# Kernel optimization log

Measured on AMD Instinct MI355X. Metric: run time of the kernel, lower is better.

## Reference

```python
import jax, jax.numpy as jnp
import numpy as np

N_NODES = 100000
N_EDGES = 1600000
IN_DIM, HID_DIM, N_CLASSES = 128, 64, 40


def spmm(edge_row, edge_col, edge_val, dense):
    # sparse [N,N] @ dense [N,D] via gather + segment-sum over edges
    msgs = edge_val[:, None] * dense[edge_col]            # [E, D]
    return jax.ops.segment_sum(msgs, edge_row, num_segments=N_NODES)


def setup_inputs() -> dict:
    key = jax.random.key(0)
    ks = jax.random.split(key, 8)
    x = jax.random.normal(ks[0], (N_NODES, IN_DIM), dtype=jnp.float32)
    edge_row = jax.random.randint(ks[1], (N_EDGES,), 0, N_NODES, dtype=jnp.int32)
    edge_col = jax.random.randint(ks[2], (N_EDGES,), 0, N_NODES, dtype=jnp.int32)
    edge_val = jax.random.uniform(ks[3], (N_EDGES,), dtype=jnp.float32)
    s1 = 1.0 / np.sqrt(IN_DIM)
    s2 = 1.0 / np.sqrt(HID_DIM)
    W1 = jax.random.normal(ks[4], (IN_DIM, HID_DIM), dtype=jnp.float32) * s1
    b1 = jnp.zeros((HID_DIM,), dtype=jnp.float32)
    W2 = jax.random.normal(ks[5], (HID_DIM, HID_DIM), dtype=jnp.float32) * s2
    b2 = jnp.zeros((HID_DIM,), dtype=jnp.float32)
    Wc = jax.random.normal(ks[6], (HID_DIM, N_CLASSES), dtype=jnp.float32) * s2
    bc = jnp.zeros((N_CLASSES,), dtype=jnp.float32)
    return {"x": x, "edge_row": edge_row, "edge_col": edge_col, "edge_val": edge_val,
            "W1": W1, "b1": b1, "W2": W2, "b2": b2, "Wc": Wc, "bc": bc}


def reference(x, edge_row, edge_col, edge_val, W1, b1, W2, b2, Wc, bc):
    # GCN layer 1: support = xW+b, aggregate, relu  (dropout off in eval)
    h = jax.nn.relu(spmm(edge_row, edge_col, edge_val, x @ W1 + b1))
    # GCN layer 2
    h = spmm(edge_row, edge_col, edge_val, h @ W2 + b2)
    # node classifier + log-softmax
    logits = h @ Wc + bc
    return jax.nn.log_softmax(logits, axis=-1)
```

## Files before the change

### kernel.cpp

```cpp
#include <hip/hip_runtime.h>

#define N_NODES   100000
#define N_EDGES   1600000
#define IN_DIM    128
#define HID_DIM   64
#define N_CLASSES 40

#define NBUCK 782
#define BCAP  2816
#define EPB   6400
#define PBLK  1024

typedef __attribute__((ext_vector_type(8))) short bf16x8;
typedef __attribute__((ext_vector_type(4))) float f32x4;

__device__ inline short f2bf(float f) {
    unsigned u = __float_as_uint(f);
    unsigned r = (u + 0x7FFFu + ((u >> 16) & 1u)) >> 16;
    return (short)r;
}
__device__ inline float bflo(unsigned w) { return __uint_as_float(w << 16); }
__device__ inline float bfhi(unsigned w) { return __uint_as_float(w & 0xFFFF0000u); }
__device__ inline float upval(unsigned w) { return __uint_as_float((w >> 17) << 16); }

__global__ __launch_bounds__(256) void prep_weights(const float* __restrict__ W1,
                                                    const float* __restrict__ W2,
                                                    const float* __restrict__ Wc,
                                                    const float* __restrict__ b2,
                                                    short* __restrict__ W1t,
                                                    short* __restrict__ Mt,
                                                    float* __restrict__ bv,
                                                    int* __restrict__ bcnt) {
    for (int i = blockIdx.x * 256 + threadIdx.x; i < IN_DIM * HID_DIM; i += gridDim.x * 256) {
        int n = i >> 7, k = i & 127;
        W1t[i] = f2bf(W1[k * HID_DIM + n]);
    }
    if (blockIdx.x == 7) {
        for (int i = threadIdx.x; i < NBUCK; i += 256) bcnt[i] = 0;
    }
    if (blockIdx.x == 0) {
        for (int idx = threadIdx.x; idx < HID_DIM * HID_DIM; idx += 256) {
            int n = idx >> 6, i = idx & 63;
            float acc = 0.f;
            if (n < N_CLASSES)
                for (int j = 0; j < HID_DIM; ++j)
                    acc = fmaf(W2[i * HID_DIM + j], Wc[j * N_CLASSES + n], acc);
            Mt[n * HID_DIM + i] = f2bf(acc);
        }
        for (int n = threadIdx.x; n < N_CLASSES; n += 256) {
            float acc = 0.f;
            for (int j = 0; j < HID_DIM; ++j)
                acc = fmaf(b2[j], Wc[j * N_CLASSES + n], acc);
            bv[n] = acc;
        }
    }
}

__global__ __launch_bounds__(256) void gemm1_mfma(const float* __restrict__ x,
                                                  const short* __restrict__ W1t,
                                                  const float* __restrict__ b1,
                                                  unsigned short* __restrict__ out) {
    int wave = threadIdx.x >> 6;
    int lane = threadIdx.x & 63;
    int node0 = blockIdx.x * 64 + wave * 16;
    if (node0 >= N_NODES) return;
    int m = lane & 15;
    int q = lane >> 4;
    const float* xrow = x + (size_t)(node0 + m) * IN_DIM;
    f32x4 acc0 = {0,0,0,0}, acc1 = {0,0,0,0}, acc2 = {0,0,0,0}, acc3 = {0,0,0,0};
#pragma unroll
    for (int kb = 0; kb < 4; ++kb) {
        int k0 = kb * 32 + q * 8;
        float4 a0 = *(const float4*)(xrow + k0);
        float4 a1 = *(const float4*)(xrow + k0 + 4);
        bf16x8 af;
        af[0]=f2bf(a0.x); af[1]=f2bf(a0.y); af[2]=f2bf(a0.z); af[3]=f2bf(a0.w);
        af[4]=f2bf(a1.x); af[5]=f2bf(a1.y); af[6]=f2bf(a1.z); af[7]=f2bf(a1.w);
        bf16x8 bf0 = *(const bf16x8*)(W1t + ( 0 + m) * IN_DIM + k0);
        bf16x8 bf1 = *(const bf16x8*)(W1t + (16 + m) * IN_DIM + k0);
        bf16x8 bf2 = *(const bf16x8*)(W1t + (32 + m) * IN_DIM + k0);
        bf16x8 bf3 = *(const bf16x8*)(W1t + (48 + m) * IN_DIM + k0);
        acc0 = __builtin_amdgcn_mfma_f32_16x16x32_bf16(af, bf0, acc0, 0, 0, 0);
        acc1 = __builtin_amdgcn_mfma_f32_16x16x32_bf16(af, bf1, acc1, 0, 0, 0);
        acc2 = __builtin_amdgcn_mfma_f32_16x16x32_bf16(af, bf2, acc2, 0, 0, 0);
        acc3 = __builtin_amdgcn_mfma_f32_16x16x32_bf16(af, bf3, acc3, 0, 0, 0);
    }
    f32x4 accs[4] = {acc0, acc1, acc2, acc3};
#pragma unroll
    for (int t = 0; t < 4; ++t) {
        float bias = b1[t * 16 + m];
#pragma unroll
        for (int r = 0; r < 4; ++r) {
            int node = node0 + q * 4 + r;
            out[(size_t)node * HID_DIM + t * 16 + m] = (unsigned short)f2bf(accs[t][r] + bias);
        }
    }
}

__global__ __launch_bounds__(256) void gemm2u_mfma(const unsigned short* __restrict__ h,
                                                   const short* __restrict__ Mt,
                                                   unsigned short* __restrict__ out) {
    int wave = threadIdx.x >> 6;
    int lane = threadIdx.x & 63;
    int node0 = blockIdx.x * 64 + wave * 16;
    if (node0 >= N_NODES) return;
    int m = lane & 15;
    int q = lane >> 4;
    const unsigned short* hrow = h + (size_t)(node0 + m) * HID_DIM;
    f32x4 acc0 = {0,0,0,0}, acc1 = {0,0,0,0}, acc2 = {0,0,0,0}, acc3 = {0,0,0,0};
#pragma unroll
    for (int kb = 0; kb < 2; ++kb) {
        int k0 = kb * 32 + q * 8;
        bf16x8 af = *(const bf16x8*)(hrow + k0);
#pragma unroll
        for (int j = 0; j < 8; ++j)
            af[j] = ((unsigned short)af[j] & 0x8000u) ? 0 : af[j];
        bf16x8 bf0 = *(const bf16x8*)(Mt + ( 0 + m) * HID_DIM + k0);
        bf16x8 bf1 = *(const bf16x8*)(Mt + (16 + m) * HID_DIM + k0);
        bf16x8 bf2 = *(const bf16x8*)(Mt + (32 + m) * HID_DIM + k0);
        bf16x8 bf3 = *(const bf16x8*)(Mt + (48 + m) * HID_DIM + k0);
        acc0 = __builtin_amdgcn_mfma_f32_16x16x32_bf16(af, bf0, acc0, 0, 0, 0);
        acc1 = __builtin_amdgcn_mfma_f32_16x16x32_bf16(af, bf1, acc1, 0, 0, 0);
        acc2 = __builtin_amdgcn_mfma_f32_16x16x32_bf16(af, bf2, acc2, 0, 0, 0);
        acc3 = __builtin_amdgcn_mfma_f32_16x16x32_bf16(af, bf3, acc3, 0, 0, 0);
    }
    f32x4 accs[4] = {acc0, acc1, acc2, acc3};
#pragma unroll
    for (int t = 0; t < 4; ++t) {
#pragma unroll
        for (int r = 0; r < 4; ++r) {
            int node = node0 + q * 4 + r;
            out[(size_t)node * HID_DIM + t * 16 + m] = (unsigned short)f2bf(accs[t][r]);
        }
    }
}

__global__ __launch_bounds__(PBLK) void part_a(const int* __restrict__ erow,
                                               const int* __restrict__ ecol,
                                               const float* __restrict__ eval,
                                               int* __restrict__ bcnt,
                                               int2* __restrict__ tmp) {
    __shared__ int2 pay[EPB];
    __shared__ unsigned short sbuck[EPB];
    __shared__ int hist[NBUCK], lbase[NBUCK], cur[NBUCK], dofs[NBUCK], scan[NBUCK];
    int e0 = blockIdx.x * EPB;
    int tid = threadIdx.x;
    for (int i = tid; i < NBUCK; i += PBLK) { hist[i] = 0; cur[i] = 0; }
    __syncthreads();
    for (int i = tid; i < EPB; i += PBLK)
        atomicAdd(&hist[erow[e0 + i] >> 7], 1);
    __syncthreads();
    for (int i = tid; i < NBUCK; i += PBLK) {
        int n = hist[i];
        dofs[i] = i * BCAP + (n ? atomicAdd(&bcnt[i], n) : 0);
        scan[i] = n;
    }
    __syncthreads();
    for (int off = 1; off < NBUCK; off <<= 1) {
        int t = 0;
        if (tid < NBUCK && tid >= off) t = scan[tid - off];
        __syncthreads();
        if (tid < NBUCK) scan[tid] += t;
        __syncthreads();
    }
    if (tid < NBUCK) {
        lbase[tid] = scan[tid] - hist[tid];
        dofs[tid] -= lbase[tid];
    }
    __syncthreads();
    for (int i = tid; i < EPB; i += PBLK) {
        int e = e0 + i;
        int r = erow[e];
        int b = r >> 7;
        int p = lbase[b] + atomicAdd(&cur[b], 1);
        pay[p] = make_int2(((r & 127) << 17) | ecol[e], __float_as_int(eval[e]));
        sbuck[p] = (unsigned short)b;
    }
    __syncthreads();
    for (int p = tid; p < EPB; p += PBLK) {
        int b = sbuck[p];
        int dest = dofs[b] + p;
        if (dest < (b + 1) * BCAP)
            tmp[dest] = pay[p];
    }
}

__global__ __launch_bounds__(256) void part_b(const int* __restrict__ bcnt,
                                              const int2* __restrict__ tmp,
                                              unsigned* __restrict__ tmp2,
                                              int2* __restrict__ rowmeta) {
    __shared__ int2 ein[BCAP];
    __shared__ unsigned eout[BCAP];
    __shared__ int hist[128], pad[128], basep[128], cur[128], scan[128];
    int b = blockIdx.x;
    int nb = bcnt[b]; if (nb > BCAP) nb = BCAP;
    for (int i = threadIdx.x; i < nb; i += 256) ein[i] = tmp[(size_t)b * BCAP + i];
    if (threadIdx.x < 128) { hist[threadIdx.x] = 0; cur[threadIdx.x] = 0; }
    __syncthreads();
    for (int i = threadIdx.x; i < nb; i += 256)
        atomicAdd(&hist[(ein[i].x >> 17) & 127], 1);
    __syncthreads();
    if (threadIdx.x < 128) {
        pad[threadIdx.x] = (hist[threadIdx.x] + 7) & ~7;
        scan[threadIdx.x] = pad[threadIdx.x];
    }
    __syncthreads();
    for (int off = 1; off < 128; off <<= 1) {
        int t = 0;
        if (threadIdx.x < 128 && threadIdx.x >= off) t = scan[threadIdx.x - off];
        __syncthreads();
        if (threadIdx.x < 128) scan[threadIdx.x] += t;
        __syncthreads();
    }
    if (threadIdx.x < 128) basep[threadIdx.x] = scan[threadIdx.x] - pad[threadIdx.x];
    __syncthreads();
    int ntot = scan[127]; if (ntot > BCAP) ntot = BCAP;
    for (int i = threadIdx.x; i < nb; i += 256) {
        int lr = (ein[i].x >> 17) & 127;
        int p = basep[lr] + atomicAdd(&cur[lr], 1);
        if (p < BCAP) {
            unsigned u = (unsigned)ein[i].y;
            unsigned vb = ((u + 0x7FFFu + ((u >> 16) & 1u)) >> 16) & 0x7FFFu;
            eout[p] = (vb << 17) | (unsigned)(ein[i].x & 0x1FFFF);
        }
    }
    __syncthreads();
    if (threadIdx.x < 128) {
        int pe = basep[threadIdx.x] + pad[threadIdx.x];
        for (int p = basep[threadIdx.x] + hist[threadIdx.x]; p < pe && p < BCAP; ++p)
            eout[p] = 0u;
    }
    __syncthreads();
    for (int i = threadIdx.x; i < ntot; i += 256) tmp2[(size_t)b * BCAP + i] = eout[i];
    if (threadIdx.x < 128) {
        int r = b * 128 + threadIdx.x;
        if (r < N_NODES)
            rowmeta[r] = make_int2(b * BCAP + basep[threadIdx.x], pad[threadIdx.x]);
    }
}

__global__ __launch_bounds__(256) void spmm_csr(const int2* __restrict__ rowmeta,
                                                const unsigned* __restrict__ ecv,
                                                const unsigned short* __restrict__ dense,
                                                unsigned short* __restrict__ out) {
    __shared__ unsigned lm[4][8][68];
    int wave = threadIdx.x >> 6;
    int lane = threadIdx.x & 63;
    int s = lane >> 3, dq = lane & 7;
    int r = (blockIdx.x * 4 + wave) * 8 + s;
    int2 meta = rowmeta[r];
    int beg = meta.x, deg = meta.y;
    int degc = deg < 64 ? deg : 64;
    for (int e = dq; e < degc; e += 8)
        lm[wave][s][e] = ecv[beg + e];
    __syncthreads();
    const unsigned* mp = lm[wave][s];
    float a0=0,a1=0,a2=0,a3=0,a4=0,a5=0,a6=0,a7=0;
    if (deg > 0) {
        uint4 w = *(const uint4*)mp;
        for (int e = 0; e < degc; e += 4) {
            uint4 wn = (e + 4 < degc) ? *(const uint4*)(mp + e + 4) : w;
            uint4 g0 = *(const uint4*)(dense + ((size_t)(w.x & 0x1FFFF) << 6) + (dq << 3));
            uint4 g1 = *(const uint4*)(dense + ((size_t)(w.y & 0x1FFFF) << 6) + (dq << 3));
            uint4 g2 = *(const uint4*)(dense + ((size_t)(w.z & 0x1FFFF) << 6) + (dq << 3));
            uint4 g3 = *(const uint4*)(dense + ((size_t)(w.w & 0x1FFFF) << 6) + (dq << 3));
            float v0 = upval(w.x), v1 = upval(w.y), v2 = upval(w.z), v3 = upval(w.w);
            a0=fmaf(v0,bflo(g0.x),a0); a1=fmaf(v0,bfhi(g0.x),a1); a2=fmaf(v0,bflo(g0.y),a2); a3=fmaf(v0,bfhi(g0.y),a3);
            a4=fmaf(v0,bflo(g0.z),a4); a5=fmaf(v0,bfhi(g0.z),a5); a6=fmaf(v0,bflo(g0.w),a6); a7=fmaf(v0,bfhi(g0.w),a7);
            a0=fmaf(v1,bflo(g1.x),a0); a1=fmaf(v1,bfhi(g1.x),a1); a2=fmaf(v1,bflo(g1.y),a2); a3=fmaf(v1,bfhi(g1.y),a3);
            a4=fmaf(v1,bflo(g1.z),a4); a5=fmaf(v1,bfhi(g1.z),a5); a6=fmaf(v1,bflo(g1.w),a6); a7=fmaf(v1,bfhi(g1.w),a7);
            a0=fmaf(v2,bflo(g2.x),a0); a1=fmaf(v2,bfhi(g2.x),a1); a2=fmaf(v2,bflo(g2.y),a2); a3=fmaf(v2,bfhi(g2.y),a3);
            a4=fmaf(v2,bflo(g2.z),a4); a5=fmaf(v2,bfhi(g2.z),a5); a6=fmaf(v2,bflo(g2.w),a6); a7=fmaf(v2,bfhi(g2.w),a7);
            a0=fmaf(v3,bflo(g3.x),a0); a1=fmaf(v3,bfhi(g3.x),a1); a2=fmaf(v3,bflo(g3.y),a2); a3=fmaf(v3,bfhi(g3.y),a3);
            a4=fmaf(v3,bflo(g3.z),a4); a5=fmaf(v3,bfhi(g3.z),a5); a6=fmaf(v3,bflo(g3.w),a6); a7=fmaf(v3,bfhi(g3.w),a7);
            w = wn;
        }
        for (int e = 64; e < deg; ++e) {
            unsigned we = ecv[beg + e];
            uint4 g = *(const uint4*)(dense + ((size_t)(we & 0x1FFFF) << 6) + (dq << 3));
            float v = upval(we);
            a0=fmaf(v,bflo(g.x),a0); a1=fmaf(v,bfhi(g.x),a1); a2=fmaf(v,bflo(g.y),a2); a3=fmaf(v,bfhi(g.y),a3);
            a4=fmaf(v,bflo(g.z),a4); a5=fmaf(v,bfhi(g.z),a5); a6=fmaf(v,bflo(g.w),a6); a7=fmaf(v,bfhi(g.w),a7);
        }
    }
    uint4 o;
    o.x = (unsigned short)f2bf(a0) | ((unsigned)(unsigned short)f2bf(a1) << 16);
    o.y = (unsigned short)f2bf(a2) | ((unsigned)(unsigned short)f2bf(a3) << 16);
    o.z = (unsigned short)f2bf(a4) | ((unsigned)(unsigned short)f2bf(a5) << 16);
    o.w = (unsigned short)f2bf(a6) | ((unsigned)(unsigned short)f2bf(a7) << 16);
    *(uint4*)(out + (size_t)r * HID_DIM + (dq << 3)) = o;
}

__global__ __launch_bounds__(256) void spmm_cls(const int2* __restrict__ rowmeta,
                                                const unsigned* __restrict__ ecv,
                                                const unsigned short* __restrict__ dense,
                                                const float* __restrict__ bv,
                                                const float* __restrict__ bc,
                                                float* __restrict__ outF) {
    __shared__ unsigned lm[4][8][68];
    int wave = threadIdx.x >> 6;
    int lane = threadIdx.x & 63;
    int s = lane >> 3, dq = lane & 7;
    int r = (blockIdx.x * 4 + wave) * 8 + s;
    float4 bv0 = {0,0,0,0}, bv1 = {0,0,0,0}, bc0 = {0,0,0,0}, bc1 = {0,0,0,0};
    if (dq < 5) {
        bv0 = *(const float4*)(bv + dq * 8);  bv1 = *(const float4*)(bv + dq * 8 + 4);
        bc0 = *(const float4*)(bc + dq * 8);  bc1 = *(const float4*)(bc + dq * 8 + 4);
    }
    int2 meta = rowmeta[r];
    int beg = meta.x, deg = meta.y;
    int degc = deg < 64 ? deg : 64;
    for (int e = dq; e < degc; e += 8)
        lm[wave][s][e] = ecv[beg + e];
    __syncthreads();
    const unsigned* mp = lm[wave][s];
    float a0=0,a1=0,a2=0,a3=0,a4=0,a5=0,a6=0,a7=0, asum=0;
    if (deg > 0) {
        uint4 w = *(const uint4*)mp;
        for (int e = 0; e < degc; e += 4) {
            uint4 wn = (e + 4 < degc) ? *(const uint4*)(mp + e + 4) : w;
            uint4 g0 = *(const uint4*)(dense + ((size_t)(w.x & 0x1FFFF) << 6) + (dq << 3));
            uint4 g1 = *(const uint4*)(dense + ((size_t)(w.y & 0x1FFFF) << 6) + (dq << 3));
            uint4 g2 = *(const uint4*)(dense + ((size_t)(w.z & 0x1FFFF) << 6) + (dq << 3));
            uint4 g3 = *(const uint4*)(dense + ((size_t)(w.w & 0x1FFFF) << 6) + (dq << 3));
            float v0 = upval(w.x), v1 = upval(w.y), v2 = upval(w.z), v3 = upval(w.w);
            asum += v0 + v1 + v2 + v3;
            a0=fmaf(v0,bflo(g0.x),a0); a1=fmaf(v0,bfhi(g0.x),a1); a2=fmaf(v0,bflo(g0.y),a2); a3=fmaf(v0,bfhi(g0.y),a3);
            a4=fmaf(v0,bflo(g0.z),a4); a5=fmaf(v0,bfhi(g0.z),a5); a6=fmaf(v0,bflo(g0.w),a6); a7=fmaf(v0,bfhi(g0.w),a7);
            a0=fmaf(v1,bflo(g1.x),a0); a1=fmaf(v1,bfhi(g1.x),a1); a2=fmaf(v1,bflo(g1.y),a2); a3=fmaf(v1,bfhi(g1.y),a3);
            a4=fmaf(v1,bflo(g1.z),a4); a5=fmaf(v1,bfhi(g1.z),a5); a6=fmaf(v1,bflo(g1.w),a6); a7=fmaf(v1,bfhi(g1.w),a7);
            a0=fmaf(v2,bflo(g2.x),a0); a1=fmaf(v2,bfhi(g2.x),a1); a2=fmaf(v2,bflo(g2.y),a2); a3=fmaf(v2,bfhi(g2.y),a3);
            a4=fmaf(v2,bflo(g2.z),a4); a5=fmaf(v2,bfhi(g2.z),a5); a6=fmaf(v2,bflo(g2.w),a6); a7=fmaf(v2,bfhi(g2.w),a7);
            a0=fmaf(v3,bflo(g3.x),a0); a1=fmaf(v3,bfhi(g3.x),a1); a2=fmaf(v3,bflo(g3.y),a2); a3=fmaf(v3,bfhi(g3.y),a3);
            a4=fmaf(v3,bflo(g3.z),a4); a5=fmaf(v3,bfhi(g3.z),a5); a6=fmaf(v3,bflo(g3.w),a6); a7=fmaf(v3,bfhi(g3.w),a7);
            w = wn;
        }
        for (int e = 64; e < deg; ++e) {
            unsigned we = ecv[beg + e];
            uint4 g = *(const uint4*)(dense + ((size_t)(we & 0x1FFFF) << 6) + (dq << 3));
            float v = upval(we);
            asum += v;
            a0=fmaf(v,bflo(g.x),a0); a1=fmaf(v,bfhi(g.x),a1); a2=fmaf(v,bflo(g.y),a2); a3=fmaf(v,bfhi(g.y),a3);
            a4=fmaf(v,bflo(g.z),a4); a5=fmaf(v,bfhi(g.z),a5); a6=fmaf(v,bflo(g.w),a6); a7=fmaf(v,bfhi(g.w),a7);
        }
    }
    float l0 = fmaf(asum, bv0.x, a0) + bc0.x;
    float l1 = fmaf(asum, bv0.y, a1) + bc0.y;
    float l2 = fmaf(asum, bv0.z, a2) + bc0.z;
    float l3 = fmaf(asum, bv0.w, a3) + bc0.w;
    float l4 = fmaf(asum, bv1.x, a4) + bc1.x;
    float l5 = fmaf(asum, bv1.y, a5) + bc1.y;
    float l6 = fmaf(asum, bv1.z, a6) + bc1.z;
    float l7 = fmaf(asum, bv1.w, a7) + bc1.w;
    float mx = -1e30f;
    if (dq < 5)
        mx = fmaxf(fmaxf(fmaxf(l0, l1), fmaxf(l2, l3)),
                   fmaxf(fmaxf(l4, l5), fmaxf(l6, l7)));
#pragma unroll
    for (int off = 1; off < 8; off <<= 1) mx = fmaxf(mx, __shfl_xor(mx, off));
    float ss = 0.f;
    if (dq < 5)
        ss = __expf(l0 - mx) + __expf(l1 - mx) + __expf(l2 - mx) + __expf(l3 - mx)
           + __expf(l4 - mx) + __expf(l5 - mx) + __expf(l6 - mx) + __expf(l7 - mx);
#pragma unroll
    for (int off = 1; off < 8; off <<= 1) ss += __shfl_xor(ss, off);
    float lse = mx + __logf(ss);
    if (dq < 5) {
        float4 o0 = {l0 - lse, l1 - lse, l2 - lse, l3 - lse};
        float4 o1 = {l4 - lse, l5 - lse, l6 - lse, l7 - lse};
        float* dst = outF + (size_t)r * N_CLASSES + dq * 8;
        *(float4*)(dst) = o0;
        *(float4*)(dst + 4) = o1;
    }
}

extern "C" void kernel_launch(void* const* d_in, const int* in_sizes, int n_in,
                              void* d_out, int out_size, void* d_ws, size_t ws_size,
                              hipStream_t stream) {
    const float* x    = (const float*)d_in[0];
    const int*   erow = (const int*)  d_in[1];
    const int*   ecol = (const int*)  d_in[2];
    const float* eval = (const float*)d_in[3];
    const float* W1   = (const float*)d_in[4];
    const float* b1   = (const float*)d_in[5];
    const float* W2   = (const float*)d_in[6];
    const float* b2   = (const float*)d_in[7];
    const float* Wc   = (const float*)d_in[8];
    const float* bc   = (const float*)d_in[9];
    float* out = (float*)d_out;

    char* ws = (char*)d_ws;
    size_t off = 0;
    auto alloc = [&](size_t bytes) { char* p = ws + off; off += (bytes + 255) & ~(size_t)255; return p; };
    unsigned short* bufA = (unsigned short*)alloc((size_t)N_NODES * HID_DIM * sizeof(short));
    unsigned short* bufB = (unsigned short*)alloc((size_t)N_NODES * HID_DIM * sizeof(short));
    int2*     tmp     = (int2*)    alloc((size_t)NBUCK * BCAP * sizeof(int2));
    unsigned* tmp2    = (unsigned*)alloc((size_t)NBUCK * BCAP * sizeof(unsigned));
    int2*     rowmeta = (int2*)    alloc((size_t)N_NODES * sizeof(int2));
    int*      bcnt    = (int*)     alloc(NBUCK * sizeof(int));
    short*    W1t     = (short*)   alloc((size_t)IN_DIM * HID_DIM * sizeof(short));
    short*    Mt      = (short*)   alloc((size_t)HID_DIM * HID_DIM * sizeof(short));
    float*    bv      = (float*)   alloc(64 * sizeof(float));

    const int tile_grid = (N_NODES + 63) / 64;
    const int spmm_grid = N_NODES / 32;
    const int grid_a    = (N_EDGES + EPB - 1) / EPB;

    prep_weights<<<8, 256, 0, stream>>>(W1, W2, Wc, b2, W1t, Mt, bv, bcnt);
    part_a<<<grid_a, PBLK, 0, stream>>>(erow, ecol, eval, bcnt, tmp);
    part_b<<<NBUCK, 256, 0, stream>>>(bcnt, tmp, tmp2, rowmeta);

    gemm1_mfma<<<tile_grid, 256, 0, stream>>>(x, W1t, b1, bufA);
    spmm_csr<<<spmm_grid, 256, 0, stream>>>(rowmeta, tmp2, bufA, bufB);
    gemm2u_mfma<<<tile_grid, 256, 0, stream>>>(bufB, Mt, bufA);
    spmm_cls<<<spmm_grid, 256, 0, stream>>>(rowmeta, tmp2, bufA, bv, bc, out);
}
```

Before: 268.1 us.

## Fuse bucket-sort second pass with first GEMM into one launch

```diff
diff --git a/kernel.cpp b/kernel.cpp
--- a/kernel.cpp
+++ b/kernel.cpp
@@ -10,6 +10,7 @@
 #define BCAP  2816
 #define EPB   6400
 #define PBLK  1024
+#define G1BLK 1563
 
 typedef __attribute__((ext_vector_type(8))) short bf16x8;
 typedef __attribute__((ext_vector_type(4))) float f32x4;
@@ -56,43 +57,149 @@
     }
 }
 
-__global__ __launch_bounds__(256) void gemm1_mfma(const float* __restrict__ x,
-                                                  const short* __restrict__ W1t,
-                                                  const float* __restrict__ b1,
-                                                  unsigned short* __restrict__ out) {
-    int wave = threadIdx.x >> 6;
-    int lane = threadIdx.x & 63;
-    int node0 = blockIdx.x * 64 + wave * 16;
-    if (node0 >= N_NODES) return;
-    int m = lane & 15;
-    int q = lane >> 4;
-    const float* xrow = x + (size_t)(node0 + m) * IN_DIM;
-    f32x4 acc0 = {0,0,0,0}, acc1 = {0,0,0,0}, acc2 = {0,0,0,0}, acc3 = {0,0,0,0};
-#pragma unroll
-    for (int kb = 0; kb < 4; ++kb) {
-        int k0 = kb * 32 + q * 8;
-        float4 a0 = *(const float4*)(xrow + k0);
-        float4 a1 = *(const float4*)(xrow + k0 + 4);
-        bf16x8 af;
-        af[0]=f2bf(a0.x); af[1]=f2bf(a0.y); af[2]=f2bf(a0.z); af[3]=f2bf(a0.w);
-        af[4]=f2bf(a1.x); af[5]=f2bf(a1.y); af[6]=f2bf(a1.z); af[7]=f2bf(a1.w);
-        bf16x8 bf0 = *(const bf16x8*)(W1t + ( 0 + m) * IN_DIM + k0);
-        bf16x8 bf1 = *(const bf16x8*)(W1t + (16 + m) * IN_DIM + k0);
-        bf16x8 bf2 = *(const bf16x8*)(W1t + (32 + m) * IN_DIM + k0);
-        bf16x8 bf3 = *(const bf16x8*)(W1t + (48 + m) * IN_DIM + k0);
-        acc0 = __builtin_amdgcn_mfma_f32_16x16x32_bf16(af, bf0, acc0, 0, 0, 0);
-        acc1 = __builtin_amdgcn_mfma_f32_16x16x32_bf16(af, bf1, acc1, 0, 0, 0);
-        acc2 = __builtin_amdgcn_mfma_f32_16x16x32_bf16(af, bf2, acc2, 0, 0, 0);
-        acc3 = __builtin_amdgcn_mfma_f32_16x16x32_bf16(af, bf3, acc3, 0, 0, 0);
-    }
-    f32x4 accs[4] = {acc0, acc1, acc2, acc3};
-#pragma unroll
-    for (int t = 0; t < 4; ++t) {
-        float bias = b1[t * 16 + m];
-#pragma unroll
-        for (int r = 0; r < 4; ++r) {
-            int node = node0 + q * 4 + r;
-            out[(size_t)node * HID_DIM + t * 16 + m] = (unsigned short)f2bf(accs[t][r] + bias);
+__global__ __launch_bounds__(PBLK) void part_a(const int* __restrict__ erow,
+                                               const int* __restrict__ ecol,
+                                               const float* __restrict__ eval,
+                                               int* __restrict__ bcnt,
+                                               int2* __restrict__ tmp) {
+    __shared__ int2 pay[EPB];
+    __shared__ int hist[NBUCK], lbase[NBUCK], cur[NBUCK], dofs[NBUCK], scan[NBUCK];
+    int e0 = blockIdx.x * EPB;
+    int tid = threadIdx.x;
+    for (int i = tid; i < NBUCK; i += PBLK) { hist[i] = 0; cur[i] = 0; }
+    __syncthreads();
+    for (int i = tid; i < EPB; i += PBLK)
+        atomicAdd(&hist[erow[e0 + i] >> 7], 1);
+    __syncthreads();
+    for (int i = tid; i < NBUCK; i += PBLK) {
+        int n = hist[i];
+        dofs[i] = i * BCAP + (n ? atomicAdd(&bcnt[i], n) : 0);
+        scan[i] = n;
+    }
+    __syncthreads();
+    for (int off = 1; off < NBUCK; off <<= 1) {
+        int t = 0;
+        if (tid < NBUCK && tid >= off) t = scan[tid - off];
+        __syncthreads();
+        if (tid < NBUCK) scan[tid] += t;
+        __syncthreads();
+    }
+    if (tid < NBUCK) {
+        lbase[tid] = scan[tid] - hist[tid];
+        dofs[tid] -= lbase[tid];
+    }
+    __syncthreads();
+    for (int i = tid; i < EPB; i += PBLK) {
+        int e = e0 + i;
+        int r = erow[e];
+        int b = r >> 7;
+        int p = lbase[b] + atomicAdd(&cur[b], 1);
+        unsigned u = __float_as_uint(eval[e]);
+        unsigned vb = ((u + 0x7FFFu + ((u >> 16) & 1u)) >> 16) & 0x7FFFu;
+        pay[p] = make_int2(((r & 127) << 17) | ecol[e], (int)((vb << 10) | (unsigned)b));
+    }
+    __syncthreads();
+    for (int p = tid; p < EPB; p += PBLK) {
+        int2 v = pay[p];
+        int b = (unsigned)v.y & 1023u;
+        int dest = dofs[b] + p;
+        if (dest < (b + 1) * BCAP)
+            tmp[dest] = v;
+    }
+}
+
+__global__ __launch_bounds__(256) void part_b_gemm1(const int* __restrict__ bcnt,
+                                                    const int2* __restrict__ tmp,
+                                                    unsigned* __restrict__ tmp2,
+                                                    int2* __restrict__ rowmeta,
+                                                    const float* __restrict__ x,
+                                                    const short* __restrict__ W1t,
+                                                    const float* __restrict__ b1,
+                                                    unsigned short* __restrict__ outH) {
+    __shared__ int2 ein[BCAP];
+    __shared__ unsigned eout[BCAP];
+    __shared__ int hist[128], pad[128], basep[128], cur[128], scan[128];
+    if (blockIdx.x < NBUCK) {
+        int b = blockIdx.x;
+        int nb = bcnt[b]; if (nb > BCAP) nb = BCAP;
+        for (int i = threadIdx.x; i < nb; i += 256) ein[i] = tmp[(size_t)b * BCAP + i];
+        if (threadIdx.x < 128) { hist[threadIdx.x] = 0; cur[threadIdx.x] = 0; }
+        __syncthreads();
+        for (int i = threadIdx.x; i < nb; i += 256)
+            atomicAdd(&hist[(ein[i].x >> 17) & 127], 1);
+        __syncthreads();
+        if (threadIdx.x < 128) {
+            pad[threadIdx.x] = (hist[threadIdx.x] + 3) & ~3;
+            scan[threadIdx.x] = pad[threadIdx.x];
+        }
+        __syncthreads();
+        for (int off = 1; off < 128; off <<= 1) {
+            int t = 0;
+            if (threadIdx.x < 128 && threadIdx.x >= off) t = scan[threadIdx.x - off];
+            __syncthreads();
+            if (threadIdx.x < 128) scan[threadIdx.x] += t;
+            __syncthreads();
+        }
+        if (threadIdx.x < 128) basep[threadIdx.x] = scan[threadIdx.x] - pad[threadIdx.x];
+        __syncthreads();
+        int ntot = scan[127]; if (ntot > BCAP) ntot = BCAP;
+        for (int i = threadIdx.x; i < nb; i += 256) {
+            int lr = (ein[i].x >> 17) & 127;
+            int p = basep[lr] + atomicAdd(&cur[lr], 1);
+            if (p < BCAP) {
+                unsigned vb = ((unsigned)ein[i].y >> 10) & 0x7FFFu;
+                eout[p] = (vb << 17) | (unsigned)(ein[i].x & 0x1FFFF);
+            }
+        }
+        __syncthreads();
+        if (threadIdx.x < 128) {
+            int pe = basep[threadIdx.x] + pad[threadIdx.x];
+            for (int p = basep[threadIdx.x] + hist[threadIdx.x]; p < pe && p < BCAP; ++p)
+                eout[p] = 0u;
+        }
+        __syncthreads();
+        for (int i = threadIdx.x; i < ntot; i += 256) tmp2[(size_t)b * BCAP + i] = eout[i];
+        if (threadIdx.x < 128) {
+            int r = b * 128 + threadIdx.x;
+            if (r < N_NODES)
+                rowmeta[r] = make_int2(b * BCAP + basep[threadIdx.x], pad[threadIdx.x]);
+        }
+    } else {
+        int gb = blockIdx.x - NBUCK;
+        int wave = threadIdx.x >> 6;
+        int lane = threadIdx.x & 63;
+        int node0 = gb * 64 + wave * 16;
+        if (node0 >= N_NODES) return;
+        int m = lane & 15;
+        int q = lane >> 4;
+        const float* xrow = x + (size_t)(node0 + m) * IN_DIM;
+        f32x4 acc0 = {0,0,0,0}, acc1 = {0,0,0,0}, acc2 = {0,0,0,0}, acc3 = {0,0,0,0};
+#pragma unroll
+        for (int kb = 0; kb < 4; ++kb) {
+            int k0 = kb * 32 + q * 8;
+            float4 a0 = *(const float4*)(xrow + k0);
+            float4 a1 = *(const float4*)(xrow + k0 + 4);
+            bf16x8 af;
+            af[0]=f2bf(a0.x); af[1]=f2bf(a0.y); af[2]=f2bf(a0.z); af[3]=f2bf(a0.w);
+            af[4]=f2bf(a1.x); af[5]=f2bf(a1.y); af[6]=f2bf(a1.z); af[7]=f2bf(a1.w);
+            bf16x8 bf0 = *(const bf16x8*)(W1t + ( 0 + m) * IN_DIM + k0);
+            bf16x8 bf1 = *(const bf16x8*)(W1t + (16 + m) * IN_DIM + k0);
+            bf16x8 bf2 = *(const bf16x8*)(W1t + (32 + m) * IN_DIM + k0);
+            bf16x8 bf3 = *(const bf16x8*)(W1t + (48 + m) * IN_DIM + k0);
+            acc0 = __builtin_amdgcn_mfma_f32_16x16x32_bf16(af, bf0, acc0, 0, 0, 0);
+            acc1 = __builtin_amdgcn_mfma_f32_16x16x32_bf16(af, bf1, acc1, 0, 0, 0);
+            acc2 = __builtin_amdgcn_mfma_f32_16x16x32_bf16(af, bf2, acc2, 0, 0, 0);
+            acc3 = __builtin_amdgcn_mfma_f32_16x16x32_bf16(af, bf3, acc3, 0, 0, 0);
+        }
+        f32x4 accs[4] = {acc0, acc1, acc2, acc3};
+#pragma unroll
+        for (int t = 0; t < 4; ++t) {
+            float bias = b1[t * 16 + m];
+#pragma unroll
+            for (int r = 0; r < 4; ++r) {
+                int node = node0 + q * 4 + r;
+                outH[(size_t)node * HID_DIM + t * 16 + m] = (unsigned short)f2bf(accs[t][r] + bias);
+            }
         }
     }
 }
@@ -132,110 +239,6 @@
             int node = node0 + q * 4 + r;
             out[(size_t)node * HID_DIM + t * 16 + m] = (unsigned short)f2bf(accs[t][r]);
         }
-    }
-}
-
-__global__ __launch_bounds__(PBLK) void part_a(const int* __restrict__ erow,
-                                               const int* __restrict__ ecol,
-                                               const float* __restrict__ eval,
-                                               int* __restrict__ bcnt,
-                                               int2* __restrict__ tmp) {
-    __shared__ int2 pay[EPB];
-    __shared__ unsigned short sbuck[EPB];
-    __shared__ int hist[NBUCK], lbase[NBUCK], cur[NBUCK], dofs[NBUCK], scan[NBUCK];
-    int e0 = blockIdx.x * EPB;
-    int tid = threadIdx.x;
-    for (int i = tid; i < NBUCK; i += PBLK) { hist[i] = 0; cur[i] = 0; }
-    __syncthreads();
-    for (int i = tid; i < EPB; i += PBLK)
-        atomicAdd(&hist[erow[e0 + i] >> 7], 1);
-    __syncthreads();
-    for (int i = tid; i < NBUCK; i += PBLK) {
-        int n = hist[i];
-        dofs[i] = i * BCAP + (n ? atomicAdd(&bcnt[i], n) : 0);
-        scan[i] = n;
-    }
-    __syncthreads();
-    for (int off = 1; off < NBUCK; off <<= 1) {
-        int t = 0;
-        if (tid < NBUCK && tid >= off) t = scan[tid - off];
-        __syncthreads();
-        if (tid < NBUCK) scan[tid] += t;
-        __syncthreads();
-    }
-    if (tid < NBUCK) {
-        lbase[tid] = scan[tid] - hist[tid];
-        dofs[tid] -= lbase[tid];
-    }
-    __syncthreads();
-    for (int i = tid; i < EPB; i += PBLK) {
-        int e = e0 + i;
-        int r = erow[e];
-        int b = r >> 7;
-        int p = lbase[b] + atomicAdd(&cur[b], 1);
-        pay[p] = make_int2(((r & 127) << 17) | ecol[e], __float_as_int(eval[e]));
-        sbuck[p] = (unsigned short)b;
-    }
-    __syncthreads();
-    for (int p = tid; p < EPB; p += PBLK) {
-        int b = sbuck[p];
-        int dest = dofs[b] + p;
-        if (dest < (b + 1) * BCAP)
-            tmp[dest] = pay[p];
-    }
-}
-
-__global__ __launch_bounds__(256) void part_b(const int* __restrict__ bcnt,
-                                              const int2* __restrict__ tmp,
-                                              unsigned* __restrict__ tmp2,
-                                              int2* __restrict__ rowmeta) {
-    __shared__ int2 ein[BCAP];
-    __shared__ unsigned eout[BCAP];
-    __shared__ int hist[128], pad[128], basep[128], cur[128], scan[128];
-    int b = blockIdx.x;
-    int nb = bcnt[b]; if (nb > BCAP) nb = BCAP;
-    for (int i = threadIdx.x; i < nb; i += 256) ein[i] = tmp[(size_t)b * BCAP + i];
-    if (threadIdx.x < 128) { hist[threadIdx.x] = 0; cur[threadIdx.x] = 0; }
-    __syncthreads();
-    for (int i = threadIdx.x; i < nb; i += 256)
-        atomicAdd(&hist[(ein[i].x >> 17) & 127], 1);
-    __syncthreads();
-    if (threadIdx.x < 128) {
-        pad[threadIdx.x] = (hist[threadIdx.x] + 7) & ~7;
-        scan[threadIdx.x] = pad[threadIdx.x];
-    }
-    __syncthreads();
-    for (int off = 1; off < 128; off <<= 1) {
-        int t = 0;
-        if (threadIdx.x < 128 && threadIdx.x >= off) t = scan[threadIdx.x - off];
-        __syncthreads();
-        if (threadIdx.x < 128) scan[threadIdx.x] += t;
-        __syncthreads();
-    }
-    if (threadIdx.x < 128) basep[threadIdx.x] = scan[threadIdx.x] - pad[threadIdx.x];
-    __syncthreads();
-    int ntot = scan[127]; if (ntot > BCAP) ntot = BCAP;
-    for (int i = threadIdx.x; i < nb; i += 256) {
-        int lr = (ein[i].x >> 17) & 127;
-        int p = basep[lr] + atomicAdd(&cur[lr], 1);
-        if (p < BCAP) {
-            unsigned u = (unsigned)ein[i].y;
-            unsigned vb = ((u + 0x7FFFu + ((u >> 16) & 1u)) >> 16) & 0x7FFFu;
-            eout[p] = (vb << 17) | (unsigned)(ein[i].x & 0x1FFFF);
-        }
-    }
-    __syncthreads();
-    if (threadIdx.x < 128) {
-        int pe = basep[threadIdx.x] + pad[threadIdx.x];
-        for (int p = basep[threadIdx.x] + hist[threadIdx.x]; p < pe && p < BCAP; ++p)
-            eout[p] = 0u;
-    }
-    __syncthreads();
-    for (int i = threadIdx.x; i < ntot; i += 256) tmp2[(size_t)b * BCAP + i] = eout[i];
-    if (threadIdx.x < 128) {
-        int r = b * 128 + threadIdx.x;
-        if (r < N_NODES)
-            rowmeta[r] = make_int2(b * BCAP + basep[threadIdx.x], pad[threadIdx.x]);
     }
 }
 
@@ -408,9 +411,8 @@
 
     prep_weights<<<8, 256, 0, stream>>>(W1, W2, Wc, b2, W1t, Mt, bv, bcnt);
     part_a<<<grid_a, PBLK, 0, stream>>>(erow, ecol, eval, bcnt, tmp);
-    part_b<<<NBUCK, 256, 0, stream>>>(bcnt, tmp, tmp2, rowmeta);
-
-    gemm1_mfma<<<tile_grid, 256, 0, stream>>>(x, W1t, b1, bufA);
+    part_b_gemm1<<<NBUCK + tile_grid, 256, 0, stream>>>(bcnt, tmp, tmp2, rowmeta,
+                                                        x, W1t, b1, bufA);
     spmm_csr<<<spmm_grid, 256, 0, stream>>>(rowmeta, tmp2, bufA, bufB);
     gemm2u_mfma<<<tile_grid, 256, 0, stream>>>(bufB, Mt, bufA);
     spmm_cls<<<spmm_grid, 256, 0, stream>>>(rowmeta, tmp2, bufA, bv, bc, out);
```

New measurement: 262.1 us. 2.3% less time.
